# Kernel optimization log

Hardware: AMD Instinct MI355X
Metric: run time of the kernel (lower is better)

The kernel has to match this reference:

```python
import jax, jax.numpy as jnp
import numpy as np

N = 30000
NUM_FEAT = 129   # data.x.shape[1] + 1
NUM_CLASSES = 40
HID = 64

def _gat_conv(x, src, dst, W, a_src, a_dst, bias):
    """PyG GATConv (concat=True, negative_slope=0.2), self-loops pre-added to src/dst."""
    n = x.shape[0]
    H, C = a_src.shape
    h = (x @ W).reshape(n, H, C)                       # [N,H,C]
    alpha_s = jnp.sum(h * a_src[None], axis=-1)        # [N,H]
    alpha_d = jnp.sum(h * a_dst[None], axis=-1)        # [N,H]
    e = jax.nn.leaky_relu(alpha_s[src] + alpha_d[dst], 0.2)   # [E,H]
    m = jax.ops.segment_max(e, dst, num_segments=n)
    m = jnp.where(jnp.isfinite(m), m, 0.0)
    ex = jnp.exp(e - m[dst])
    denom = jax.ops.segment_sum(ex, dst, num_segments=n)
    alpha = ex / (denom[dst] + 1e-16)                  # segment softmax over in-edges
    out = jax.ops.segment_sum(h[src] * alpha[:, :, None], dst, num_segments=n)
    return out.reshape(n, H * C) + bias


def setup_inputs() -> dict:
    key = jax.random.key(0)
    ks = jax.random.split(key, 16)
    E = 480000
    x = jax.random.normal(ks[0], (N, NUM_FEAT), dtype=jnp.float32)
    edge_index = jax.random.randint(ks[1], (2, E), 0, N, dtype=jnp.int64)
    def w(k, shape, fan_in):
        return (jax.random.normal(k, shape, dtype=jnp.float32) * (1.0 / np.sqrt(fan_in))).astype(jnp.float32)
    # conv1: in=129, H=7, C=64
    W1 = w(ks[2], (NUM_FEAT, 7 * HID), NUM_FEAT)
    a1s = w(ks[3], (7, HID), HID); a1d = w(ks[4], (7, HID), HID)
    b1 = jnp.zeros((7 * HID,), jnp.float32)
    # conv2: in=448, H=6, C=64
    W2 = w(ks[5], (7 * HID, 6 * HID), 7 * HID)
    a2s = w(ks[6], (6, HID), HID); a2d = w(ks[7], (6, HID), HID)
    b2 = jnp.zeros((6 * HID,), jnp.float32)
    # conv3: in=384, H=6, C=40
    W3 = w(ks[8], (6 * HID, 6 * NUM_CLASSES), 6 * HID)
    a3s = w(ks[9], (6, NUM_CLASSES), NUM_CLASSES); a3d = w(ks[10], (6, NUM_CLASSES), NUM_CLASSES)
    b3 = jnp.zeros((6 * NUM_CLASSES,), jnp.float32)
    return {"x": x, "edge_index": edge_index,
            "W1": W1, "a1s": a1s, "a1d": a1d, "b1": b1,
            "W2": W2, "a2s": a2s, "a2d": a2d, "b2": b2,
            "W3": W3, "a3s": a3s, "a3d": a3d, "b3": b3}


def reference(x, edge_index, W1, a1s, a1d, b1, W2, a2s, a2d, b2, W3, a3s, a3d, b3):
    n = x.shape[0]
    loop = jnp.arange(n, dtype=edge_index.dtype)
    src = jnp.concatenate([edge_index[0], loop])   # PyG add_self_loops=True
    dst = jnp.concatenate([edge_index[1], loop])
    # dropout is identity in eval mode
    h = _gat_conv(x, src, dst, W1, a1s, a1d, b1)
    h = jax.nn.relu(h)
    h = _gat_conv(h, src, dst, W2, a2s, a2d, b2)
    h = jax.nn.relu(h)
    out = _gat_conv(h, src, dst, W3, a3s, a3d, b3)
    return out
```

## Files before the change

kernel.cpp:

```cpp
#include <hip/hip_runtime.h>
#include <hip/hip_bf16.h>


#define NFEAT 129
#define MPAD  30080
#define BLKSH 11
#define KPD   16

typedef __attribute__((ext_vector_type(8))) short short8v;
typedef __attribute__((ext_vector_type(8))) unsigned short u16x8;
typedef __attribute__((ext_vector_type(8))) __bf16 bf16x8;
typedef __attribute__((ext_vector_type(4))) float f32x4;
typedef unsigned short u16;

union FragU { short8v s; bf16x8 b; };

__device__ inline u16 f2bf(float x) {
    unsigned u = __builtin_bit_cast(unsigned, x);
    unsigned r = (u + 0x7fffu + ((u >> 16) & 1u)) >> 16;
    return (u16)r;
}
__device__ inline float bf2f(u16 b) {
    unsigned u = ((unsigned)b) << 16;
    return __builtin_bit_cast(float, u);
}
__device__ inline float h2f(u16 u) { return (float)__builtin_bit_cast(_Float16, u); }
__device__ inline u16 f2h(float v) { return __builtin_bit_cast(u16, (_Float16)v); }


__global__ __launch_bounds__(256) void hist_k(const int* __restrict__ src,
                                              const int* __restrict__ dst,
                                              int* __restrict__ cnt, int E, int n) {
    int e = blockIdx.x * 256 + threadIdx.x;
    if (e < E + n) {
        int s, d;
        if (e < E) { s = src[e]; d = dst[e]; }
        else       { s = d = e - E; }
        atomicAdd(&cnt[d * KPD + (s >> BLKSH)], 1);
    }
}

__global__ __launch_bounds__(256) void bsum_k(const int* __restrict__ cnt,
                                              int* __restrict__ bsum, int nk) {
    __shared__ int sh[256];
    int t = threadIdx.x, idx = blockIdx.x * 256 + t;
    sh[t] = (idx < nk) ? cnt[idx] : 0;
    __syncthreads();
    for (int o = 128; o; o >>= 1) {
        if (t < o) sh[t] += sh[t + o];
        __syncthreads();
    }
    if (t == 0) bsum[blockIdx.x] = sh[0];
}

__global__ __launch_bounds__(1024) void bscan_k(const int* __restrict__ bsum,
                                                int* __restrict__ bofs, int nb) {
    __shared__ int part[1024];
    int t = threadIdx.x;
    int per = (nb + 1023) >> 10;
    int base = t * per;
    int s = 0;
    for (int j = 0; j < per; ++j) {
        int i = base + j;
        if (i < nb) s += bsum[i];
    }
    part[t] = s;
    __syncthreads();
    for (int o = 1; o < 1024; o <<= 1) {
        int v = 0;
        if (t >= o) v = part[t - o];
        __syncthreads();
        if (t >= o) part[t] += v;
        __syncthreads();
    }
    int run = (t > 0) ? part[t - 1] : 0;
    for (int j = 0; j < per; ++j) {
        int i = base + j;
        if (i < nb) { bofs[i] = run; run += bsum[i]; }
    }
    if (t == 1023) bofs[nb] = part[1023];
}

__global__ __launch_bounds__(256) void scanw_k(const int* __restrict__ cnt,
                                               const int* __restrict__ bofs,
                                               int* __restrict__ row_ptr, int nk) {
    __shared__ int sh[256];
    int t = threadIdx.x, idx = blockIdx.x * 256 + t;
    int v = (idx < nk) ? cnt[idx] : 0;
    sh[t] = v;
    __syncthreads();
    for (int o = 1; o < 256; o <<= 1) {
        int u = 0;
        if (t >= o) u = sh[t - o];
        __syncthreads();
        if (t >= o) sh[t] += u;
        __syncthreads();
    }
    if (idx < nk) row_ptr[idx] = bofs[blockIdx.x] + sh[t] - v;
    if (idx == nk - 1) row_ptr[nk] = bofs[blockIdx.x] + sh[t];
}

__global__ __launch_bounds__(256) void scatter_k(const int* __restrict__ src, const int* __restrict__ dst,
                                                 const int* __restrict__ row_ptr, int* __restrict__ fill,
                                                 int* __restrict__ col, int* __restrict__ dstc,
                                                 int E, int n) {
    int e = blockIdx.x * 256 + threadIdx.x;
    if (e < E + n) {
        int s, d;
        if (e < E) { s = src[e]; d = dst[e]; }
        else       { s = d = e - E; }
        int key = d * KPD + (s >> BLKSH);
        int pos = row_ptr[key] + atomicAdd(&fill[key], 1);
        col[pos] = s;
        dstc[pos] = d;
    }
}


__global__ __launch_bounds__(256) void xsplit_k(const float* __restrict__ in,
                                                u16* __restrict__ hi, u16* __restrict__ lo,
                                                int Nn, int K, int Kp, int Mp) {
    int idx = blockIdx.x * 256 + threadIdx.x;
    if (idx >= Mp * Kp) return;
    int m = idx / Kp, k = idx - m * Kp;
    float v = (m < Nn && k < K) ? in[(size_t)m * K + k] : 0.f;
    u16 h = f2bf(v);
    hi[idx] = h;
    lo[idx] = f2bf(v - bf2f(h));
}


__global__ __launch_bounds__(256) void wsplitAll_k(const float* __restrict__ W1,
                                                   const float* __restrict__ W2,
                                                   const float* __restrict__ W3,
                                                   u16* __restrict__ hi, u16* __restrict__ lo) {
    int idx = blockIdx.x * 256 + threadIdx.x;
    if (idx >= 352256) return;
    const float* W; int loc, Kp, K, N;
    if (idx < 81920)       { W = W1; loc = idx;          Kp = 160; K = 129; N = 448; }
    else if (idx < 253952) { W = W2; loc = idx - 81920;  Kp = 448; K = 448; N = 384; }
    else                   { W = W3; loc = idx - 253952; Kp = 384; K = 384; N = 240; }
    int nn = loc / Kp, k = loc - nn * Kp;
    float v = (k < K && nn < N) ? W[(size_t)k * N + nn] : 0.f;
    u16 h = f2bf(v);
    hi[idx] = h;
    lo[idx] = f2bf(v - bf2f(h));
}


__global__ __launch_bounds__(256) void projAll_k(
    const float* __restrict__ W1, const float* __restrict__ a1s, const float* __restrict__ a1d,
    const float* __restrict__ W2, const float* __restrict__ a2s, const float* __restrict__ a2d,
    const float* __restrict__ W3, const float* __restrict__ a3s, const float* __restrict__ a3d,
    float* __restrict__ Ps, float* __restrict__ Pd) {
    int idx = blockIdx.x * 256 + threadIdx.x;
    if (idx >= 992 * 8) return;
    int row = idx >> 3, h = idx & 7;
    const float *W, *as_, *ad_; int k, K, Ncols, H, C;
    if (row < 160)      { k = row;       K = 129; W = W1; as_ = a1s; ad_ = a1d; Ncols = 448; H = 7; C = 64; }
    else if (row < 608) { k = row - 160; K = 448; W = W2; as_ = a2s; ad_ = a2d; Ncols = 384; H = 6; C = 64; }
    else                { k = row - 608; K = 384; W = W3; as_ = a3s; ad_ = a3d; Ncols = 240; H = 6; C = 40; }
    float ps = 0.f, pd = 0.f;
    if (h < H && k < K) {
        const float* wr = W + (size_t)k * Ncols + h * C;
        const float* ar = as_ + h * C;
        const float* dr = ad_ + h * C;
        for (int c = 0; c < C; ++c) {
            float wv = wr[c];
            ps += wv * ar[c];
            pd += wv * dr[c];
        }
    }
    Ps[idx] = ps;
    Pd[idx] = pd;
}


__global__ __launch_bounds__(256) void zeropads_k(u16* __restrict__ hA, u16* __restrict__ hB,
                                                  int Nn) {
    int totA = (MPAD - Nn) * 448;
    int totB = (MPAD - Nn) * 384;
    int idx = blockIdx.x * 256 + threadIdx.x;
    if (idx < totA) hA[(size_t)Nn * 448 + idx] = 0;
    if (idx < totB) hB[(size_t)Nn * 384 + idx] = 0;
}


__global__ __launch_bounds__(256) void alpha1_k(const float* __restrict__ x,
                                                const float* __restrict__ Ps,
                                                const float* __restrict__ Pd,
                                                float* __restrict__ oS, float* __restrict__ oD, int n) {
    int wv = threadIdx.x >> 6, lane = threadIdx.x & 63;
    int i = blockIdx.x * 4 + wv;
    if (i >= n) return;
    const float* row = x + (size_t)i * NFEAT;
    float x0 = row[lane], x1 = row[64 + lane];
    float ps[8], pd[8];
    #pragma unroll
    for (int h = 0; h < 8; ++h) {
        ps[h] = x0 * Ps[lane * 8 + h] + x1 * Ps[(64 + lane) * 8 + h];
        pd[h] = x0 * Pd[lane * 8 + h] + x1 * Pd[(64 + lane) * 8 + h];
    }
    if (lane == 0) {
        float x2 = row[128];
        #pragma unroll
        for (int h = 0; h < 8; ++h) {
            ps[h] += x2 * Ps[128 * 8 + h];
            pd[h] += x2 * Pd[128 * 8 + h];
        }
    }
    #pragma unroll
    for (int h = 0; h < 8; ++h) {
        #pragma unroll
        for (int off = 32; off; off >>= 1) {
            ps[h] += __shfl_xor(ps[h], off);
            pd[h] += __shfl_xor(pd[h], off);
        }
    }
    if (lane == 0) {
        #pragma unroll
        for (int h = 0; h < 8; ++h) {
            oS[(size_t)i * 8 + h] = ps[h];
            oD[(size_t)i * 8 + h] = pd[h];
        }
    }
}


template <int KC>
__global__ __launch_bounds__(256) void alphaproj_k(const u16* __restrict__ H16,
                                                   const float* __restrict__ Ps,
                                                   const float* __restrict__ Pd,
                                                   float* __restrict__ oS, float* __restrict__ oD, int n) {
    constexpr int STRIDE = KC * 64;
    int wv = threadIdx.x >> 6, lane = threadIdx.x & 63;
    int i = blockIdx.x * 4 + wv;
    if (i >= n) return;
    const u16* hr = H16 + (size_t)i * STRIDE;
    float ps[8] = {}, pd[8] = {};
    #pragma unroll
    for (int kc = 0; kc < KC; ++kc) {
        int k = kc * 64 + lane;
        float v = h2f(hr[k]);
        #pragma unroll
        for (int h = 0; h < 8; ++h) {
            ps[h] += v * Ps[k * 8 + h];
            pd[h] += v * Pd[k * 8 + h];
        }
    }
    #pragma unroll
    for (int h = 0; h < 8; ++h) {
        #pragma unroll
        for (int off = 32; off; off >>= 1) {
            ps[h] += __shfl_xor(ps[h], off);
            pd[h] += __shfl_xor(pd[h], off);
        }
    }
    if (lane == 0) {
        #pragma unroll
        for (int h = 0; h < 8; ++h) {
            oS[(size_t)i * 8 + h] = ps[h];
            oD[(size_t)i * 8 + h] = pd[h];
        }
    }
}


__global__ __launch_bounds__(256) void edgew_k(const float* __restrict__ as_,
                                               const float* __restrict__ ad_,
                                               const int* __restrict__ col,
                                               const int* __restrict__ dstc,
                                               float* __restrict__ w, int Et) {
    int idx = blockIdx.x * 256 + threadIdx.x;
    if (idx >= Et * 8) return;
    int e = idx >> 3, h = idx & 7;
    int s = col[e], d = dstc[e];
    float v = as_[(size_t)s * 8 + h] + ad_[(size_t)d * 8 + h];
    v = v > 0.f ? v : 0.2f * v;
    w[idx] = __expf(v);
}


__device__ __forceinline__ int swz(int r, int s) {
    return (r << 2) | ((s ^ (r & 3) ^ ((r >> 2) & 3)) & 3);
}


template <bool ASPLIT>
__global__ __launch_bounds__(256) void gemm16(
    const u16* __restrict__ Ahi, const u16* __restrict__ Alo,
    const u16* __restrict__ A16,
    const u16* __restrict__ Bhi, const u16* __restrict__ Blo,
    u16* __restrict__ C16, int M, int Ncols, int Kp)
{
    __shared__ __align__(16) u16 sAh[128 * 32];
    __shared__ __align__(16) u16 sAl[128 * 32];
    __shared__ __align__(16) u16 sBh[128 * 32];
    __shared__ __align__(16) u16 sBl[128 * 32];
    const int tid = threadIdx.x;
    const int m0 = blockIdx.y * 128;
    const int n0 = blockIdx.x * 128;
    const int lane = tid & 63, wave = tid >> 6;
    const int wm = wave >> 1, wn = wave & 1;
    const int l15 = lane & 15, lg = lane >> 4;
    const int r0 = tid >> 2, s0 = tid & 3;
    const int w0 = swz(r0, s0), w1 = swz(r0 + 64, s0);
    f32x4 acc[4][4] = {};

    for (int k0 = 0; k0 < Kp; k0 += 32) {
        size_t gA0 = (size_t)(m0 + r0) * Kp + k0 + s0 * 8;
        size_t gA1 = (size_t)(m0 + r0 + 64) * Kp + k0 + s0 * 8;
        size_t gB0 = (size_t)(n0 + r0) * Kp + k0 + s0 * 8;
        size_t gB1 = (size_t)(n0 + r0 + 64) * Kp + k0 + s0 * 8;
        short8v ah0, ah1, al0, al1;
        if constexpr (ASPLIT) {
            ah0 = *(const short8v*)(Ahi + gA0);
            ah1 = *(const short8v*)(Ahi + gA1);
            al0 = *(const short8v*)(Alo + gA0);
            al1 = *(const short8v*)(Alo + gA1);
        } else {
            u16x8 a0 = *(const u16x8*)(A16 + gA0);
            u16x8 a1 = *(const u16x8*)(A16 + gA1);
            #pragma unroll
            for (int j = 0; j < 8; ++j) {
                float f0 = h2f(a0[j]);
                u16 h0 = f2bf(f0);
                ah0[j] = (short)h0;
                al0[j] = (short)f2bf(f0 - bf2f(h0));
                float f1 = h2f(a1[j]);
                u16 h1 = f2bf(f1);
                ah1[j] = (short)h1;
                al1[j] = (short)f2bf(f1 - bf2f(h1));
            }
        }
        short8v bh0 = *(const short8v*)(Bhi + gB0);
        short8v bh1 = *(const short8v*)(Bhi + gB1);
        short8v bl0 = *(const short8v*)(Blo + gB0);
        short8v bl1 = *(const short8v*)(Blo + gB1);
        __syncthreads();
        ((short8v*)sAh)[w0] = ah0; ((short8v*)sAh)[w1] = ah1;
        ((short8v*)sAl)[w0] = al0; ((short8v*)sAl)[w1] = al1;
        ((short8v*)sBh)[w0] = bh0; ((short8v*)sBh)[w1] = bh1;
        ((short8v*)sBl)[w0] = bl0; ((short8v*)sBl)[w1] = bl1;
        __syncthreads();
        FragU fah[4], fal[4], fbh[4], fbl[4];
        #pragma unroll
        for (int mf = 0; mf < 4; ++mf) {
            int rr = wm * 64 + mf * 16 + l15;
            int idx = swz(rr, lg);
            fah[mf].s = ((const short8v*)sAh)[idx];
            fal[mf].s = ((const short8v*)sAl)[idx];
        }
        #pragma unroll
        for (int nf = 0; nf < 4; ++nf) {
            int rr = wn * 64 + nf * 16 + l15;
            int idx = swz(rr, lg);
            fbh[nf].s = ((const short8v*)sBh)[idx];
            fbl[nf].s = ((const short8v*)sBl)[idx];
        }
        #pragma unroll
        for (int mf = 0; mf < 4; ++mf) {
            #pragma unroll
            for (int nf = 0; nf < 4; ++nf) {
                acc[mf][nf] = __builtin_amdgcn_mfma_f32_16x16x32_bf16(fah[mf].b, fbh[nf].b, acc[mf][nf], 0, 0, 0);
                acc[mf][nf] = __builtin_amdgcn_mfma_f32_16x16x32_bf16(fah[mf].b, fbl[nf].b, acc[mf][nf], 0, 0, 0);
                acc[mf][nf] = __builtin_amdgcn_mfma_f32_16x16x32_bf16(fal[mf].b, fbh[nf].b, acc[mf][nf], 0, 0, 0);
            }
        }
    }
    #pragma unroll
    for (int mf = 0; mf < 4; ++mf) {
        #pragma unroll
        for (int nf = 0; nf < 4; ++nf) {
            int colg = n0 + wn * 64 + nf * 16 + l15;
            if (colg >= Ncols) continue;
            #pragma unroll
            for (int r = 0; r < 4; ++r) {
                int rowg = m0 + wm * 64 + mf * 16 + lg * 4 + r;
                if (rowg < M) C16[(size_t)rowg * Ncols + colg] = f2h(acc[mf][nf][r]);
            }
        }
    }
}


template <int H, int C, bool RELU, bool F16OUT>
__global__ __launch_bounds__(256) void aggL_k(
    const u16* __restrict__ hf, const float* __restrict__ w,
    const float* __restrict__ bias,
    const int* __restrict__ row_ptr, const int* __restrict__ col,
    float* __restrict__ outf, u16* __restrict__ oh16, int n)
{
    constexpr int HC = H * C;
    constexpr int LACT = HC / 8;
    const int wv = threadIdx.x >> 6, lane = threadIdx.x & 63;
    const int i = blockIdx.x * 4 + wv;
    if (i >= n) return;
    const int ch0 = lane * 8;
    const bool act = lane < LACT;
    const int h = act ? (ch0 / C) : 0;
    const bool lead = act && ((ch0 % C) == 0);
    const int beg = row_ptr[i * KPD], end = row_ptr[(i + 1) * KPD];
    float acc[8] = {};
    float dp = 0.f;
    if (act) {
        int e = beg;
        for (; e + 2 <= end; e += 2) {
            int sA = col[e], sB = col[e + 1];
            float wA = w[(size_t)e * 8 + h];
            float wB = w[(size_t)(e + 1) * 8 + h];
            u16x8 vA = *(const u16x8*)(hf + (size_t)sA * HC + ch0);
            u16x8 vB = *(const u16x8*)(hf + (size_t)sB * HC + ch0);
            #pragma unroll
            for (int j = 0; j < 8; ++j)
                acc[j] += wA * h2f(vA[j]) + wB * h2f(vB[j]);
            if (lead) dp += wA + wB;
        }
        if (e < end) {
            int sA = col[e];
            float wA = w[(size_t)e * 8 + h];
            u16x8 vA = *(const u16x8*)(hf + (size_t)sA * HC + ch0);
            #pragma unroll
            for (int j = 0; j < 8; ++j)
                acc[j] += wA * h2f(vA[j]);
            if (lead) dp += wA;
        }
    }
    const float den = __shfl(dp, h * (C / 8)) + 1e-16f;
    if (act) {
        float o[8];
        #pragma unroll
        for (int j = 0; j < 8; ++j) {
            float v = acc[j] / den + bias[ch0 + j];
            if (RELU) v = fmaxf(v, 0.f);
            o[j] = v;
        }
        size_t base = (size_t)i * HC + ch0;
        if constexpr (F16OUT) {
            u16x8 po;
            #pragma unroll
            for (int j = 0; j < 8; ++j) po[j] = f2h(o[j]);
            *(u16x8*)(oh16 + base) = po;
        } else {
            float4 q0; q0.x = o[0]; q0.y = o[1]; q0.z = o[2]; q0.w = o[3];
            float4 q1; q1.x = o[4]; q1.y = o[5]; q1.z = o[6]; q1.w = o[7];
            *(float4*)(outf + base) = q0;
            *(float4*)(outf + base + 4) = q1;
        }
    }
}


extern "C" void kernel_launch(void* const* d_in, const int* in_sizes, int n_in,
                              void* d_out, int out_size, void* d_ws, size_t ws_size,
                              hipStream_t stream) {
    const float* x   = (const float*)d_in[0];
    const int*   ei  = (const int*)d_in[1];
    const float* W1  = (const float*)d_in[2];
    const float* a1s = (const float*)d_in[3];
    const float* a1d = (const float*)d_in[4];
    const float* b1  = (const float*)d_in[5];
    const float* W2  = (const float*)d_in[6];
    const float* a2s = (const float*)d_in[7];
    const float* a2d = (const float*)d_in[8];
    const float* b2  = (const float*)d_in[9];
    const float* W3  = (const float*)d_in[10];
    const float* a3s = (const float*)d_in[11];
    const float* a3d = (const float*)d_in[12];
    const float* b3  = (const float*)d_in[13];
    float* out = (float*)d_out;

    const int Nn = in_sizes[0] / NFEAT;
    const int E  = in_sizes[1] / 2;
    const int Et = E + Nn;
    const int NK = Nn * KPD;
    const int NB = (NK + 255) / 256;
    const int* srcp = ei;
    const int* dstp = ei + E;

    char* ws = (char*)d_ws;
    size_t off = 0;
    auto carve = [&](size_t bytes) -> char* {
        char* p = ws + off;
        off += (bytes + 255) & ~(size_t)255;
        return p;
    };
    u16*   hbuf16 = (u16*)carve((size_t)MPAD * 448 * 2);
    u16*   hA16  = (u16*)carve((size_t)MPAD * 448 * 2);
    u16*   hB16  = (u16*)carve((size_t)MPAD * 384 * 2);
    u16*   Xhi   = (u16*)carve((size_t)MPAD * 160 * 2);
    u16*   Xlo   = (u16*)carve((size_t)MPAD * 160 * 2);
    u16*   Wthi  = (u16*)carve((size_t)352256 * 2);
    u16*   Wtlo  = (u16*)carve((size_t)352256 * 2);
    float* wbuf  = (float*)carve((size_t)Et * 8 * 4);
    int*   col   = (int*)carve((size_t)Et * 4);
    int*   dstc  = (int*)carve((size_t)Et * 4);
    int* row_ptr = (int*)carve((size_t)(NK + 1) * 4);
    int*   cnt   = (int*)carve((size_t)NK * 4);
    int*   bsum  = (int*)carve((size_t)NB * 4);
    int*   bofs  = (int*)carve((size_t)(NB + 1) * 4);
    float* aA    = (float*)carve((size_t)Nn * 8 * 4);
    float* dA    = (float*)carve((size_t)Nn * 8 * 4);
    float* aB    = (float*)carve((size_t)Nn * 8 * 4);
    float* dB    = (float*)carve((size_t)Nn * 8 * 4);
    float* Ps    = (float*)carve((size_t)992 * 8 * 4);
    float* Pd    = (float*)carve((size_t)992 * 8 * 4);
    (void)ws_size;

    const int nb4 = (Nn + 3) / 4;
    const int mg  = MPAD / 128;

    hipMemsetAsync(cnt, 0, (size_t)NK * 4, stream);
    hist_k<<<(Et + 255) / 256, 256, 0, stream>>>(srcp, dstp, cnt, E, Nn);
    bsum_k<<<NB, 256, 0, stream>>>(cnt, bsum, NK);
    bscan_k<<<1, 1024, 0, stream>>>(bsum, bofs, NB);
    scanw_k<<<NB, 256, 0, stream>>>(cnt, bofs, row_ptr, NK);
    hipMemsetAsync(cnt, 0, (size_t)NK * 4, stream);
    scatter_k<<<(Et + 255) / 256, 256, 0, stream>>>(srcp, dstp, row_ptr, cnt, col, dstc, E, Nn);

    xsplit_k<<<((MPAD * 160) + 255) / 256, 256, 0, stream>>>(x, Xhi, Xlo, Nn, NFEAT, 160, MPAD);
    wsplitAll_k<<<(352256 + 255) / 256, 256, 0, stream>>>(W1, W2, W3, Wthi, Wtlo);
    projAll_k<<<(992 * 8 + 255) / 256, 256, 0, stream>>>(W1, a1s, a1d, W2, a2s, a2d, W3, a3s, a3d, Ps, Pd);
    zeropads_k<<<(((MPAD - Nn) * 448) + 255) / 256, 256, 0, stream>>>(hA16, hB16, Nn);

    alpha1_k<<<nb4, 256, 0, stream>>>(x, Ps, Pd, aA, dA, Nn);
    edgew_k<<<(Et * 8 + 255) / 256, 256, 0, stream>>>(aA, dA, col, dstc, wbuf, Et);
    gemm16<true><<<dim3(4, mg), 256, 0, stream>>>(Xhi, Xlo, nullptr, Wthi, Wtlo,
                                                  hbuf16, Nn, 448, 160);
    aggL_k<7, 64, true, true><<<nb4, 256, 0, stream>>>(
        hbuf16, wbuf, b1, row_ptr, col, nullptr, hA16, Nn);
    alphaproj_k<7><<<nb4, 256, 0, stream>>>(hA16, Ps + 1280, Pd + 1280, aB, dB, Nn);

    edgew_k<<<(Et * 8 + 255) / 256, 256, 0, stream>>>(aB, dB, col, dstc, wbuf, Et);
    gemm16<false><<<dim3(3, mg), 256, 0, stream>>>(nullptr, nullptr, hA16,
                                                   Wthi + 81920, Wtlo + 81920,
                                                   hbuf16, Nn, 384, 448);
    aggL_k<6, 64, true, true><<<nb4, 256, 0, stream>>>(
        hbuf16, wbuf, b2, row_ptr, col, nullptr, hB16, Nn);
    alphaproj_k<6><<<nb4, 256, 0, stream>>>(hB16, Ps + 4864, Pd + 4864, aA, dA, Nn);

    edgew_k<<<(Et * 8 + 255) / 256, 256, 0, stream>>>(aA, dA, col, dstc, wbuf, Et);
    gemm16<false><<<dim3(2, mg), 256, 0, stream>>>(nullptr, nullptr, hB16,
                                                   Wthi + 253952, Wtlo + 253952,
                                                   hbuf16, Nn, 240, 384);
    aggL_k<6, 40, false, false><<<nb4, 256, 0, stream>>>(
        hbuf16, wbuf, b3, row_ptr, col, out, nullptr, Nn);
}
```

Baseline: 494.9 us.

## Use plain per-destination CSR and merge prep kernels into one launch

The edge sort key changes from (dst, src-block) buckets, with 16 buckets per node, to plain destination rows. This shrinks the histogram, scan and row_ptr arrays sixteenfold and cuts scan work, but it drops the source-block ordering that likely gave the gather in aggregation better locality. The four preprocessing kernels (x split, W split, projection, zero padding) are fused into a single launch to save launch overhead. The fused kernel hardcodes N=30000 when sizing the pad regions.

After: 492.6 us. Within noise of the previous version (-0.5%).

```diff
diff --git a/kernel.cpp b/kernel.cpp
--- a/kernel.cpp
+++ b/kernel.cpp
@@ -4,8 +4,6 @@
 
 #define NFEAT 129
 #define MPAD  30080
-#define BLKSH 11
-#define KPD   16
 
 typedef __attribute__((ext_vector_type(8))) short short8v;
 typedef __attribute__((ext_vector_type(8))) unsigned short u16x8;
@@ -28,15 +26,12 @@
 __device__ inline u16 f2h(float v) { return __builtin_bit_cast(u16, (_Float16)v); }
 
 
-__global__ __launch_bounds__(256) void hist_k(const int* __restrict__ src,
-                                              const int* __restrict__ dst,
+__global__ __launch_bounds__(256) void hist_k(const int* __restrict__ dst,
                                               int* __restrict__ cnt, int E, int n) {
     int e = blockIdx.x * 256 + threadIdx.x;
     if (e < E + n) {
-        int s, d;
-        if (e < E) { s = src[e]; d = dst[e]; }
-        else       { s = d = e - E; }
-        atomicAdd(&cnt[d * KPD + (s >> BLKSH)], 1);
+        int d = (e < E) ? dst[e] : (e - E);
+        atomicAdd(&cnt[d], 1);
     }
 }
 
@@ -109,80 +104,71 @@
         int s, d;
         if (e < E) { s = src[e]; d = dst[e]; }
         else       { s = d = e - E; }
-        int key = d * KPD + (s >> BLKSH);
-        int pos = row_ptr[key] + atomicAdd(&fill[key], 1);
+        int pos = row_ptr[d] + atomicAdd(&fill[d], 1);
         col[pos] = s;
         dstc[pos] = d;
     }
 }
 
 
-__global__ __launch_bounds__(256) void xsplit_k(const float* __restrict__ in,
-                                                u16* __restrict__ hi, u16* __restrict__ lo,
-                                                int Nn, int K, int Kp, int Mp) {
-    int idx = blockIdx.x * 256 + threadIdx.x;
-    if (idx >= Mp * Kp) return;
-    int m = idx / Kp, k = idx - m * Kp;
-    float v = (m < Nn && k < K) ? in[(size_t)m * K + k] : 0.f;
-    u16 h = f2bf(v);
-    hi[idx] = h;
-    lo[idx] = f2bf(v - bf2f(h));
-}
-
-
-__global__ __launch_bounds__(256) void wsplitAll_k(const float* __restrict__ W1,
-                                                   const float* __restrict__ W2,
-                                                   const float* __restrict__ W3,
-                                                   u16* __restrict__ hi, u16* __restrict__ lo) {
-    int idx = blockIdx.x * 256 + threadIdx.x;
-    if (idx >= 352256) return;
-    const float* W; int loc, Kp, K, N;
-    if (idx < 81920)       { W = W1; loc = idx;          Kp = 160; K = 129; N = 448; }
-    else if (idx < 253952) { W = W2; loc = idx - 81920;  Kp = 448; K = 448; N = 384; }
-    else                   { W = W3; loc = idx - 253952; Kp = 384; K = 384; N = 240; }
-    int nn = loc / Kp, k = loc - nn * Kp;
-    float v = (k < K && nn < N) ? W[(size_t)k * N + nn] : 0.f;
-    u16 h = f2bf(v);
-    hi[idx] = h;
-    lo[idx] = f2bf(v - bf2f(h));
-}
-
-
-__global__ __launch_bounds__(256) void projAll_k(
+__global__ __launch_bounds__(256) void prep_k(
+    const float* __restrict__ x,
     const float* __restrict__ W1, const float* __restrict__ a1s, const float* __restrict__ a1d,
     const float* __restrict__ W2, const float* __restrict__ a2s, const float* __restrict__ a2d,
     const float* __restrict__ W3, const float* __restrict__ a3s, const float* __restrict__ a3d,
-    float* __restrict__ Ps, float* __restrict__ Pd) {
+    u16* __restrict__ Xhi, u16* __restrict__ Xlo,
+    u16* __restrict__ Whi, u16* __restrict__ Wlo,
+    float* __restrict__ Ps, float* __restrict__ Pd,
+    u16* __restrict__ hA, u16* __restrict__ hB, int Nn)
+{
+    const int S1 = MPAD * 160;
+    const int S2 = S1 + 352256;
+    const int S3 = S2 + 992 * 8;
+    const int S4 = S3 + (MPAD - 30000) * 448;
+    const int S5 = S4 + (MPAD - 30000) * 384;
     int idx = blockIdx.x * 256 + threadIdx.x;
-    if (idx >= 992 * 8) return;
-    int row = idx >> 3, h = idx & 7;
-    const float *W, *as_, *ad_; int k, K, Ncols, H, C;
-    if (row < 160)      { k = row;       K = 129; W = W1; as_ = a1s; ad_ = a1d; Ncols = 448; H = 7; C = 64; }
-    else if (row < 608) { k = row - 160; K = 448; W = W2; as_ = a2s; ad_ = a2d; Ncols = 384; H = 6; C = 64; }
-    else                { k = row - 608; K = 384; W = W3; as_ = a3s; ad_ = a3d; Ncols = 240; H = 6; C = 40; }
-    float ps = 0.f, pd = 0.f;
-    if (h < H && k < K) {
-        const float* wr = W + (size_t)k * Ncols + h * C;
-        const float* ar = as_ + h * C;
-        const float* dr = ad_ + h * C;
-        for (int c = 0; c < C; ++c) {
-            float wv = wr[c];
-            ps += wv * ar[c];
-            pd += wv * dr[c];
-        }
-    }
-    Ps[idx] = ps;
-    Pd[idx] = pd;
-}
-
-
-__global__ __launch_bounds__(256) void zeropads_k(u16* __restrict__ hA, u16* __restrict__ hB,
-                                                  int Nn) {
-    int totA = (MPAD - Nn) * 448;
-    int totB = (MPAD - Nn) * 384;
-    int idx = blockIdx.x * 256 + threadIdx.x;
-    if (idx < totA) hA[(size_t)Nn * 448 + idx] = 0;
-    if (idx < totB) hB[(size_t)Nn * 384 + idx] = 0;
+    if (idx < S1) {
+        int m = idx / 160, k = idx - m * 160;
+        float v = (m < Nn && k < NFEAT) ? x[(size_t)m * NFEAT + k] : 0.f;
+        u16 h = f2bf(v);
+        Xhi[idx] = h;
+        Xlo[idx] = f2bf(v - bf2f(h));
+    } else if (idx < S2) {
+        int loc0 = idx - S1;
+        const float* W; int loc, Kp, K, N;
+        if (loc0 < 81920)       { W = W1; loc = loc0;          Kp = 160; K = 129; N = 448; }
+        else if (loc0 < 253952) { W = W2; loc = loc0 - 81920;  Kp = 448; K = 448; N = 384; }
+        else                    { W = W3; loc = loc0 - 253952; Kp = 384; K = 384; N = 240; }
+        int nn = loc / Kp, k = loc - nn * Kp;
+        float v = (k < K && nn < N) ? W[(size_t)k * N + nn] : 0.f;
+        u16 h = f2bf(v);
+        Whi[loc0] = h;
+        Wlo[loc0] = f2bf(v - bf2f(h));
+    } else if (idx < S3) {
+        int loc0 = idx - S2;
+        int row = loc0 >> 3, h = loc0 & 7;
+        const float *W, *as_, *ad_; int k, K, Ncols, H, C;
+        if (row < 160)      { k = row;       K = 129; W = W1; as_ = a1s; ad_ = a1d; Ncols = 448; H = 7; C = 64; }
+        else if (row < 608) { k = row - 160; K = 448; W = W2; as_ = a2s; ad_ = a2d; Ncols = 384; H = 6; C = 64; }
+        else                { k = row - 608; K = 384; W = W3; as_ = a3s; ad_ = a3d; Ncols = 240; H = 6; C = 40; }
+        float ps = 0.f, pd = 0.f;
+        if (h < H && k < K) {
+            const float* wr = W + (size_t)k * Ncols + h * C;
+            const float* ar = as_ + h * C;
+            const float* dr = ad_ + h * C;
+            for (int c = 0; c < C; ++c) {
+                float wv = wr[c];
+                ps += wv * ar[c];
+                pd += wv * dr[c];
+            }
+        }
+        Ps[loc0] = ps;
+        Pd[loc0] = pd;
+    } else if (idx < S4) {
+        hA[(size_t)Nn * 448 + (idx - S3)] = 0;
+    } else if (idx < S5) {
+        hB[(size_t)Nn * 384 + (idx - S4)] = 0;
+    }
 }
 
 
@@ -400,7 +386,7 @@
     const bool act = lane < LACT;
     const int h = act ? (ch0 / C) : 0;
     const bool lead = act && ((ch0 % C) == 0);
-    const int beg = row_ptr[i * KPD], end = row_ptr[(i + 1) * KPD];
+    const int beg = row_ptr[i], end = row_ptr[i + 1];
     float acc[8] = {};
     float dp = 0.f;
     if (act) {
@@ -473,8 +459,7 @@
     const int Nn = in_sizes[0] / NFEAT;
     const int E  = in_sizes[1] / 2;
     const int Et = E + Nn;
-    const int NK = Nn * KPD;
-    const int NB = (NK + 255) / 256;
+    const int NB = (Nn + 255) / 256;
     const int* srcp = ei;
     const int* dstp = ei + E;
 
@@ -495,8 +480,8 @@
     float* wbuf  = (float*)carve((size_t)Et * 8 * 4);
     int*   col   = (int*)carve((size_t)Et * 4);
     int*   dstc  = (int*)carve((size_t)Et * 4);
-    int* row_ptr = (int*)carve((size_t)(NK + 1) * 4);
-    int*   cnt   = (int*)carve((size_t)NK * 4);
+    int* row_ptr = (int*)carve((size_t)(Nn + 1) * 4);
+    int*   cnt   = (int*)carve((size_t)Nn * 4);
     int*   bsum  = (int*)carve((size_t)NB * 4);
     int*   bofs  = (int*)carve((size_t)(NB + 1) * 4);
     float* aA    = (float*)carve((size_t)Nn * 8 * 4);
@@ -509,19 +494,19 @@
 
     const int nb4 = (Nn + 3) / 4;
     const int mg  = MPAD / 128;
-
-    hipMemsetAsync(cnt, 0, (size_t)NK * 4, stream);
-    hist_k<<<(Et + 255) / 256, 256, 0, stream>>>(srcp, dstp, cnt, E, Nn);
-    bsum_k<<<NB, 256, 0, stream>>>(cnt, bsum, NK);
+    const int PREP_TOT = MPAD * 160 + 352256 + 992 * 8 + (MPAD - 30000) * 448 + (MPAD - 30000) * 384;
+
+    hipMemsetAsync(cnt, 0, (size_t)Nn * 4, stream);
+    hist_k<<<(Et + 255) / 256, 256, 0, stream>>>(dstp, cnt, E, Nn);
+    bsum_k<<<NB, 256, 0, stream>>>(cnt, bsum, Nn);
     bscan_k<<<1, 1024, 0, stream>>>(bsum, bofs, NB);
-    scanw_k<<<NB, 256, 0, stream>>>(cnt, bofs, row_ptr, NK);
-    hipMemsetAsync(cnt, 0, (size_t)NK * 4, stream);
+    scanw_k<<<NB, 256, 0, stream>>>(cnt, bofs, row_ptr, Nn);
+    hipMemsetAsync(cnt, 0, (size_t)Nn * 4, stream);
     scatter_k<<<(Et + 255) / 256, 256, 0, stream>>>(srcp, dstp, row_ptr, cnt, col, dstc, E, Nn);
 
-    xsplit_k<<<((MPAD * 160) + 255) / 256, 256, 0, stream>>>(x, Xhi, Xlo, Nn, NFEAT, 160, MPAD);
-    wsplitAll_k<<<(352256 + 255) / 256, 256, 0, stream>>>(W1, W2, W3, Wthi, Wtlo);
-    projAll_k<<<(992 * 8 + 255) / 256, 256, 0, stream>>>(W1, a1s, a1d, W2, a2s, a2d, W3, a3s, a3d, Ps, Pd);
-    zeropads_k<<<(((MPAD - Nn) * 448) + 255) / 256, 256, 0, stream>>>(hA16, hB16, Nn);
+    prep_k<<<(PREP_TOT + 255) / 256, 256, 0, stream>>>(
+        x, W1, a1s, a1d, W2, a2s, a2d, W3, a3s, a3d,
+        Xhi, Xlo, Wthi, Wtlo, Ps, Pd, hA16, hB16, Nn);
 
     alpha1_k<<<nb4, 256, 0, stream>>>(x, Ps, Pd, aA, dA, Nn);
     edgew_k<<<(Et * 8 + 255) / 256, 256, 0, stream>>>(aA, dA, col, dstc, wbuf, Et);
```
